# Kernel optimization log

Hardware: AMD Instinct MI355X
Metric: run time of the kernel (lower is better)

Reference implementation:

```python
import jax, jax.numpy as jnp
import numpy as np

B, L, F, R = 32, 128, 128, 4096
MAX_INTERIOR = R >> 1  # tpr.max_interior_index
N = 262144


def setup_inputs() -> dict:
    key = jax.random.key(0)
    ks = jax.random.split(key, 7)
    mem_values = jax.random.normal(ks[0], (N, F), dtype=jnp.float32)
    # zero out a slice of rows so the ConsNet pad_mask path is exercised
    mem_values = mem_values.at[: N // 20].set(0.0)
    arg_weights = jax.random.uniform(ks[1], (B, L, 4), dtype=jnp.float32)
    root_filler = jax.random.normal(ks[2], (B, F), dtype=jnp.float32)
    op_dist = jax.random.uniform(ks[3], (B, 3), dtype=jnp.float32)
    batch_idx = jax.random.randint(ks[4], (N,), 0, B, dtype=jnp.int32)
    slot_idx = jax.random.randint(ks[5], (N,), 0, L, dtype=jnp.int32)
    role_idx = jax.random.randint(ks[6], (N,), 0, R, dtype=jnp.int32)
    return {
        "mem_values": mem_values,
        "arg_weights": arg_weights,
        "root_filler": root_filler,
        "op_dist": op_dist,
        "batch_idx": batch_idx,
        "slot_idx": slot_idx,
        "role_idx": role_idx,
    }


def _forward(mem_values, arg_weights, root_filler, op_dist,
             batch_idx, slot_idx, role_idx):
    # per-entry gather of the 4 argument weights: w[n,k] = arg_weights[b_n, l_n, k]
    w = arg_weights[batch_idx, slot_idx]  # [N, 4]
    flat = batch_idx.astype(jnp.int32) * R + role_idx  # [N], coalesce key (b, r)

    def coalesce(vals):  # scatter-add == torch_sparse.coalesce into dense [B,R,F]
        g = jnp.zeros((B * R, F), vals.dtype).at[flat].add(vals)
        return g.reshape(B, R, F)

    H = R >> 1

    # ---- CarNet (sparse): weight, coalesce, keep even roles, role >>= 1 ----
    car_A = coalesce(mem_values * w[:, 0:1])            # [B,R,F]
    car_out = jnp.zeros((B, R, F), mem_values.dtype).at[:, :H].set(car_A[:, 0::2])

    # ---- CdrNet (sparse): keep odd roles != 1, role >>= 1 ----
    cdr_A = coalesce(mem_values * w[:, 1:2])
    cdr_half = cdr_A[:, 1::2]                            # roles 2r+1 -> r
    cdr_half = cdr_half.at[:, 0].set(0.0)                # exclude old role 1 (r=0)
    cdr_out = jnp.zeros((B, R, F), mem_values.dtype).at[:, :H].set(cdr_half)

    # ---- ConsNet (sparse): pad-mask weights, roles<MAX_INTERIOR, children + root ----
    pad = jnp.all(mem_values == 0, axis=1, keepdims=True)  # [N,1]
    c1 = coalesce(mem_values * jnp.where(pad, 0.0, w[:, 2:3]))
    c2 = coalesce(mem_values * jnp.where(pad, 0.0, w[:, 3:4]))
    cons_out = jnp.zeros((B, R, F), mem_values.dtype)
    cons_out = cons_out.at[:, 0::2].set(c1[:, :MAX_INTERIOR])      # r -> 2r
    cons_out = cons_out.at[:, 1::2].add(c2[:, :MAX_INTERIOR])      # r -> 2r+1
    cons_out = cons_out.at[:, 1].add(root_filler)                  # root at role 1

    # ---- op-distribution weighted combine (coalesce of the 3 streams) ----
    out = (op_dist[:, 0, None, None] * car_out
           + op_dist[:, 1, None, None] * cdr_out
           + op_dist[:, 2, None, None] * cons_out)
    return out


def reference(mem_values, arg_weights, root_filler, op_dist,
              batch_idx, slot_idx, role_idx):
    return _forward(mem_values, arg_weights, root_filler, op_dist,
                    batch_idx, slot_idx, role_idx)
```

## Files before the change

kernel.cpp:

```cpp
#include <hip/hip_runtime.h>


namespace {
constexpr int kB = 32;
constexpr int kL = 128;
constexpr int kF = 128;
constexpr int kR = 4096;
constexpr int kN = 262144;
constexpr int kNB = kB * kR;
constexpr int kCap = 32;
constexpr int kOvfMax = 4096;

constexpr size_t kOffCounts = 0;
constexpr size_t kOffOvfCnt = (size_t)kNB * 4;
constexpr size_t kOffOvf    = kOffOvfCnt + 16;
constexpr size_t kOffTokW   = 544768;
constexpr size_t kOffBuck   = kOffTokW + (size_t)kN * 16;
}

__global__ __launch_bounds__(256) void build_kernel(
    const float4* __restrict__ aw, const int* __restrict__ bidx,
    const int* __restrict__ sidx, const int* __restrict__ ridx,
    int* __restrict__ counts, int* __restrict__ ovf_cnt,
    int* __restrict__ ovf, float4* __restrict__ tokw,
    int* __restrict__ buckets) {
  int n = blockIdx.x * 256 + threadIdx.x;
  if (n >= kN) return;
  int b = bidx[n];
  int s = sidx[n];
  int rr = ridx[n];
  tokw[n] = aw[b * kL + s];
  int key = (b << 12) | rr;
  int pos = atomicAdd(&counts[key], 1);
  if (pos < kCap) {
    buckets[(size_t)key * kCap + pos] = n;
  } else {
    int o = atomicAdd(ovf_cnt, 1);
    if (o < kOvfMax) ovf[o] = n;
  }
}

__global__ __launch_bounds__(256) void gather_kernel(
    const float2* __restrict__ mem2, const float4* __restrict__ tokw,
    const float2* __restrict__ root2, const float* __restrict__ opd,
    const int* __restrict__ counts, const int* __restrict__ buckets,
    float2* __restrict__ out2) {
  const int row = blockIdx.x * 4 + (threadIdx.x >> 6);
  const int t = threadIdx.x & 63;
  const int b = row >> 12;
  const int r = row & (kR - 1);
  const float op0 = opd[3 * b + 0];
  const float op1 = opd[3 * b + 1];
  const float op2 = opd[3 * b + 2];
  float ax = 0.f, ay = 0.f;
  const int tcl = (t < kCap) ? t : (kCap - 1);

  {
    const int key = (b << 12) | (r >> 1);
    int cnt = min(counts[key], kCap);
    cnt = __builtin_amdgcn_readfirstlane(cnt);
    const int* bk = buckets + (size_t)key * kCap;
    int myidx = bk[tcl];
    const bool odd = (r & 1) != 0;
    for (int i = 0; i < cnt; ++i) {
      int n = __builtin_amdgcn_readfirstlane(__shfl(myidx, i));
      float4 w = tokw[n];
      float sc = op2 * (odd ? w.w : w.z);
      float2 m = mem2[(size_t)n * (kF / 2) + t];
      ax += sc * m.x;
      ay += sc * m.y;
    }
  }
  if (r < kR / 2) {
    {
      const int key = (b << 12) | (r << 1);
      int cnt = min(counts[key], kCap);
      cnt = __builtin_amdgcn_readfirstlane(cnt);
      const int* bk = buckets + (size_t)key * kCap;
      int myidx = bk[tcl];
      for (int i = 0; i < cnt; ++i) {
        int n = __builtin_amdgcn_readfirstlane(__shfl(myidx, i));
        float4 w = tokw[n];
        float sc = op0 * w.x;
        float2 m = mem2[(size_t)n * (kF / 2) + t];
        ax += sc * m.x;
        ay += sc * m.y;
      }
    }
    if (r >= 1) {
      const int key = (b << 12) | ((r << 1) | 1);
      int cnt = min(counts[key], kCap);
      cnt = __builtin_amdgcn_readfirstlane(cnt);
      const int* bk = buckets + (size_t)key * kCap;
      int myidx = bk[tcl];
      for (int i = 0; i < cnt; ++i) {
        int n = __builtin_amdgcn_readfirstlane(__shfl(myidx, i));
        float4 w = tokw[n];
        float sc = op1 * w.y;
        float2 m = mem2[(size_t)n * (kF / 2) + t];
        ax += sc * m.x;
        ay += sc * m.y;
      }
    }
  }
  if (r == 1) {
    float2 rf = root2[b * (kF / 2) + t];
    ax += op2 * rf.x;
    ay += op2 * rf.y;
  }
  float2 o;
  o.x = ax;
  o.y = ay;
  out2[(size_t)row * (kF / 2) + t] = o;
}

__global__ __launch_bounds__(128) void ovf_kernel(
    const float* __restrict__ mem, const float4* __restrict__ tokw,
    const float* __restrict__ opd, const int* __restrict__ bidx,
    const int* __restrict__ ridx, const int* __restrict__ ovf_cnt,
    const int* __restrict__ ovf, float* __restrict__ out) {
  int m = *ovf_cnt;
  if (m > kOvfMax) m = kOvfMax;
  const int t = threadIdx.x;
  for (int i = blockIdx.x; i < m; i += gridDim.x) {
    int n = ovf[i];
    int b = bidx[n];
    int rr = ridx[n];
    float4 w = tokw[n];
    float op0 = opd[3 * b + 0];
    float op1 = opd[3 * b + 1];
    float op2 = opd[3 * b + 2];
    float mv = mem[(size_t)n * kF + t];
    size_t base = ((size_t)b * kR) * kF;
    if ((rr & 1) == 0)
      atomicAdd(&out[base + (size_t)(rr >> 1) * kF + t], op0 * w.x * mv);
    if ((rr & 1) && rr >= 3)
      atomicAdd(&out[base + (size_t)((rr - 1) >> 1) * kF + t], op1 * w.y * mv);
    if (rr < kR / 2) {
      atomicAdd(&out[base + (size_t)(2 * rr) * kF + t], op2 * w.z * mv);
      atomicAdd(&out[base + (size_t)(2 * rr + 1) * kF + t], op2 * w.w * mv);
    }
  }
}

extern "C" void kernel_launch(void* const* d_in, const int* in_sizes, int n_in,
                              void* d_out, int out_size, void* d_ws, size_t ws_size,
                              hipStream_t stream) {
  const float* mem   = (const float*)d_in[0];
  const float* aw    = (const float*)d_in[1];
  const float* rootf = (const float*)d_in[2];
  const float* opd   = (const float*)d_in[3];
  const int* bidx    = (const int*)d_in[4];
  const int* sidx    = (const int*)d_in[5];
  const int* ridx    = (const int*)d_in[6];

  char* ws = (char*)d_ws;
  int* counts    = (int*)(ws + kOffCounts);
  int* ovf_cnt   = (int*)(ws + kOffOvfCnt);
  int* ovf       = (int*)(ws + kOffOvf);
  float4* tokw   = (float4*)(ws + kOffTokW);
  int* buckets   = (int*)(ws + kOffBuck);

  hipMemsetAsync(ws, 0, kOffOvfCnt + 4, stream);

  build_kernel<<<kN / 256, 256, 0, stream>>>(
      (const float4*)aw, bidx, sidx, ridx, counts, ovf_cnt, ovf, tokw, buckets);

  gather_kernel<<<kNB / 4, 256, 0, stream>>>(
      (const float2*)mem, tokw, (const float2*)rootf, opd, counts, buckets,
      (float2*)d_out);

  ovf_kernel<<<64, 128, 0, stream>>>(
      mem, tokw, opd, bidx, ridx, ovf_cnt, ovf, (float*)d_out);
}
```

Baseline: 321.1 us.

## Prefold op weights into token weights and batch gathers four-wide with merged bucket loads

The build kernel now multiplies each token's argument weights by the per-batch op distribution, so the gather and overflow kernels no longer load opd. The gather kernel reads the two adjacent car/cdr bucket counts and index lists with a single load. It then processes entries four at a time with predicated, independent loads, in place of a serial loop that had one outstanding load per iteration. The aim is more memory-level parallelism and lower latency per output row. The cost is wasted loads of row 0 for padded slots and extra register pressure.

```diff
diff --git a/kernel.cpp b/kernel.cpp
--- a/kernel.cpp
+++ b/kernel.cpp
@@ -19,8 +19,9 @@
 }
 
 __global__ __launch_bounds__(256) void build_kernel(
-    const float4* __restrict__ aw, const int* __restrict__ bidx,
-    const int* __restrict__ sidx, const int* __restrict__ ridx,
+    const float4* __restrict__ aw, const float* __restrict__ opd,
+    const int* __restrict__ bidx, const int* __restrict__ sidx,
+    const int* __restrict__ ridx,
     int* __restrict__ counts, int* __restrict__ ovf_cnt,
     int* __restrict__ ovf, float4* __restrict__ tokw,
     int* __restrict__ buckets) {
@@ -29,7 +30,16 @@
   int b = bidx[n];
   int s = sidx[n];
   int rr = ridx[n];
-  tokw[n] = aw[b * kL + s];
+  float4 w = aw[b * kL + s];
+  float op0 = opd[3 * b + 0];
+  float op1 = opd[3 * b + 1];
+  float op2 = opd[3 * b + 2];
+  float4 pw;
+  pw.x = w.x * op0;
+  pw.y = w.y * op1;
+  pw.z = w.z * op2;
+  pw.w = w.w * op2;
+  tokw[n] = pw;
   int key = (b << 12) | rr;
   int pos = atomicAdd(&counts[key], 1);
   if (pos < kCap) {
@@ -40,6 +50,44 @@
   }
 }
 
+template <int CH>
+__device__ __forceinline__ float pick_scale(float4 w, bool odd) {
+  if (CH == 0) return w.x;
+  if (CH == 1) return w.y;
+  return odd ? w.w : w.z;
+}
+
+template <int CH>
+__device__ __forceinline__ void proc4(int i0, int cnt, int idxvec, int laneoff,
+                                      bool odd,
+                                      const float4* __restrict__ tokw,
+                                      const float2* __restrict__ mem2, int t,
+                                      float& ax, float& ay) {
+  int n0 = __shfl(idxvec, laneoff + i0 + 0);
+  int n1 = __shfl(idxvec, laneoff + i0 + 1);
+  int n2 = __shfl(idxvec, laneoff + i0 + 2);
+  int n3 = __shfl(idxvec, laneoff + i0 + 3);
+  const bool v0 = (i0 + 0) < cnt, v1 = (i0 + 1) < cnt;
+  const bool v2 = (i0 + 2) < cnt, v3 = (i0 + 3) < cnt;
+  n0 = v0 ? n0 : 0;
+  n1 = v1 ? n1 : 0;
+  n2 = v2 ? n2 : 0;
+  n3 = v3 ? n3 : 0;
+  float4 w0 = tokw[n0], w1 = tokw[n1], w2 = tokw[n2], w3 = tokw[n3];
+  float2 m0 = mem2[(size_t)n0 * (kF / 2) + t];
+  float2 m1 = mem2[(size_t)n1 * (kF / 2) + t];
+  float2 m2 = mem2[(size_t)n2 * (kF / 2) + t];
+  float2 m3 = mem2[(size_t)n3 * (kF / 2) + t];
+  float s0 = v0 ? pick_scale<CH>(w0, odd) : 0.f;
+  float s1 = v1 ? pick_scale<CH>(w1, odd) : 0.f;
+  float s2 = v2 ? pick_scale<CH>(w2, odd) : 0.f;
+  float s3 = v3 ? pick_scale<CH>(w3, odd) : 0.f;
+  ax += s0 * m0.x; ay += s0 * m0.y;
+  ax += s1 * m1.x; ay += s1 * m1.y;
+  ax += s2 * m2.x; ay += s2 * m2.y;
+  ax += s3 * m3.x; ay += s3 * m3.y;
+}
+
 __global__ __launch_bounds__(256) void gather_kernel(
     const float2* __restrict__ mem2, const float4* __restrict__ tokw,
     const float2* __restrict__ root2, const float* __restrict__ opd,
@@ -47,64 +95,42 @@
     float2* __restrict__ out2) {
   const int row = blockIdx.x * 4 + (threadIdx.x >> 6);
   const int t = threadIdx.x & 63;
+  const int ts = t & 31;
   const int b = row >> 12;
   const int r = row & (kR - 1);
-  const float op0 = opd[3 * b + 0];
-  const float op1 = opd[3 * b + 1];
-  const float op2 = opd[3 * b + 2];
+  const bool odd = (r & 1) != 0;
+  const bool lo = r < (kR / 2);
+
+  const int keyC = (b << 12) | (r >> 1);
+  const int keyA = (b << 12) | ((r << 1) & (kR - 1));
+
+  int cntC_raw = counts[keyC];
+  int2 cntAD_raw = *(const int2*)(counts + keyA);
+  int idxC = buckets[(size_t)keyC * kCap + ts];
+  int idxAD = buckets[(size_t)keyA * kCap + t];
+
+  const int cntC = min(cntC_raw, kCap);
+  const int cntA = lo ? min(cntAD_raw.x, kCap) : 0;
+  const int cntD = (lo && r >= 1) ? min(cntAD_raw.y, kCap) : 0;
+
   float ax = 0.f, ay = 0.f;
-  const int tcl = (t < kCap) ? t : (kCap - 1);
 
-  {
-    const int key = (b << 12) | (r >> 1);
-    int cnt = min(counts[key], kCap);
-    cnt = __builtin_amdgcn_readfirstlane(cnt);
-    const int* bk = buckets + (size_t)key * kCap;
-    int myidx = bk[tcl];
-    const bool odd = (r & 1) != 0;
-    for (int i = 0; i < cnt; ++i) {
-      int n = __builtin_amdgcn_readfirstlane(__shfl(myidx, i));
-      float4 w = tokw[n];
-      float sc = op2 * (odd ? w.w : w.z);
-      float2 m = mem2[(size_t)n * (kF / 2) + t];
-      ax += sc * m.x;
-      ay += sc * m.y;
-    }
+  proc4<2>(0, cntC, idxC, 0, odd, tokw, mem2, t, ax, ay);
+  if (lo) {
+    proc4<0>(0, cntA, idxAD, 0, odd, tokw, mem2, t, ax, ay);
+    proc4<1>(0, cntD, idxAD, 32, odd, tokw, mem2, t, ax, ay);
   }
-  if (r < kR / 2) {
-    {
-      const int key = (b << 12) | (r << 1);
-      int cnt = min(counts[key], kCap);
-      cnt = __builtin_amdgcn_readfirstlane(cnt);
-      const int* bk = buckets + (size_t)key * kCap;
-      int myidx = bk[tcl];
-      for (int i = 0; i < cnt; ++i) {
-        int n = __builtin_amdgcn_readfirstlane(__shfl(myidx, i));
-        float4 w = tokw[n];
-        float sc = op0 * w.x;
-        float2 m = mem2[(size_t)n * (kF / 2) + t];
-        ax += sc * m.x;
-        ay += sc * m.y;
-      }
-    }
-    if (r >= 1) {
-      const int key = (b << 12) | ((r << 1) | 1);
-      int cnt = min(counts[key], kCap);
-      cnt = __builtin_amdgcn_readfirstlane(cnt);
-      const int* bk = buckets + (size_t)key * kCap;
-      int myidx = bk[tcl];
-      for (int i = 0; i < cnt; ++i) {
-        int n = __builtin_amdgcn_readfirstlane(__shfl(myidx, i));
-        float4 w = tokw[n];
-        float sc = op1 * w.y;
-        float2 m = mem2[(size_t)n * (kF / 2) + t];
-        ax += sc * m.x;
-        ay += sc * m.y;
-      }
-    }
-  }
+
+  for (int i = 4; i < cntC; i += 4)
+    proc4<2>(i, cntC, idxC, 0, odd, tokw, mem2, t, ax, ay);
+  for (int i = 4; i < cntA; i += 4)
+    proc4<0>(i, cntA, idxAD, 0, odd, tokw, mem2, t, ax, ay);
+  for (int i = 4; i < cntD; i += 4)
+    proc4<1>(i, cntD, idxAD, 32, odd, tokw, mem2, t, ax, ay);
+
   if (r == 1) {
     float2 rf = root2[b * (kF / 2) + t];
+    float op2 = opd[3 * b + 2];
     ax += op2 * rf.x;
     ay += op2 * rf.y;
   }
@@ -116,9 +142,9 @@
 
 __global__ __launch_bounds__(128) void ovf_kernel(
     const float* __restrict__ mem, const float4* __restrict__ tokw,
-    const float* __restrict__ opd, const int* __restrict__ bidx,
-    const int* __restrict__ ridx, const int* __restrict__ ovf_cnt,
-    const int* __restrict__ ovf, float* __restrict__ out) {
+    const int* __restrict__ bidx, const int* __restrict__ ridx,
+    const int* __restrict__ ovf_cnt, const int* __restrict__ ovf,
+    float* __restrict__ out) {
   int m = *ovf_cnt;
   if (m > kOvfMax) m = kOvfMax;
   const int t = threadIdx.x;
@@ -127,18 +153,15 @@
     int b = bidx[n];
     int rr = ridx[n];
     float4 w = tokw[n];
-    float op0 = opd[3 * b + 0];
-    float op1 = opd[3 * b + 1];
-    float op2 = opd[3 * b + 2];
     float mv = mem[(size_t)n * kF + t];
     size_t base = ((size_t)b * kR) * kF;
     if ((rr & 1) == 0)
-      atomicAdd(&out[base + (size_t)(rr >> 1) * kF + t], op0 * w.x * mv);
+      atomicAdd(&out[base + (size_t)(rr >> 1) * kF + t], w.x * mv);
     if ((rr & 1) && rr >= 3)
-      atomicAdd(&out[base + (size_t)((rr - 1) >> 1) * kF + t], op1 * w.y * mv);
+      atomicAdd(&out[base + (size_t)((rr - 1) >> 1) * kF + t], w.y * mv);
     if (rr < kR / 2) {
-      atomicAdd(&out[base + (size_t)(2 * rr) * kF + t], op2 * w.z * mv);
-      atomicAdd(&out[base + (size_t)(2 * rr + 1) * kF + t], op2 * w.w * mv);
+      atomicAdd(&out[base + (size_t)(2 * rr) * kF + t], w.z * mv);
+      atomicAdd(&out[base + (size_t)(2 * rr + 1) * kF + t], w.w * mv);
     }
   }
 }
@@ -164,12 +187,13 @@
   hipMemsetAsync(ws, 0, kOffOvfCnt + 4, stream);
 
   build_kernel<<<kN / 256, 256, 0, stream>>>(
-      (const float4*)aw, bidx, sidx, ridx, counts, ovf_cnt, ovf, tokw, buckets);
+      (const float4*)aw, opd, bidx, sidx, ridx, counts, ovf_cnt, ovf, tokw,
+      buckets);
 
   gather_kernel<<<kNB / 4, 256, 0, stream>>>(
       (const float2*)mem, tokw, (const float2*)rootf, opd, counts, buckets,
       (float2*)d_out);
 
   ovf_kernel<<<64, 128, 0, stream>>>(
-      mem, tokw, opd, bidx, ridx, ovf_cnt, ovf, (float*)d_out);
+      mem, tokw, bidx, ridx, ovf_cnt, ovf, (float*)d_out);
 }
```

Result: faster. 312.6 us (-2.7%).
